# Optimization experiments

Measured on AMD Instinct MI355X. Metric: run time of the kernel, lower is better.

Reference implementation:

```python
import jax, jax.numpy as jnp
import numpy as np

N = 50000
E = 800000
IN_CH = 128
HID = 64
HEADS = 4
NEG_SLOPE_GAT = 0.2   # PyG GATConv default negative_slope
NEG_SLOPE_ACT = 0.01  # nn.LeakyReLU default
LN_EPS = 1e-5


def segment_softmax(logits, seg, num):
    # softmax over edges grouped by destination node (PyG softmax semantics)
    m = jax.ops.segment_max(logits, seg, num_segments=num)
    m = jnp.where(jnp.isfinite(m), m, 0.0)
    e = jnp.exp(logits - m[seg])
    s = jax.ops.segment_sum(e, seg, num_segments=num)
    return e / (s[seg] + 1e-16)


def gat_conv(x, edge_index, W, a_src, a_dst, b, heads, out_ch):
    n = x.shape[0]
    loop = jnp.arange(n)
    src = jnp.concatenate([edge_index[0], loop])  # message sources (x_j)
    dst = jnp.concatenate([edge_index[1], loop])  # aggregation targets (x_i)
    h = (x @ W).reshape(n, heads, out_ch)          # [N,H,C]
    alpha_src = (h * a_src).sum(-1)                # [N,H]
    alpha_dst = (h * a_dst).sum(-1)                # [N,H]
    alpha = alpha_src[src] + alpha_dst[dst]        # [E',H]
    alpha = jax.nn.leaky_relu(alpha, NEG_SLOPE_GAT)
    alpha = segment_softmax(alpha, dst, n)
    msg = h[src] * alpha[:, :, None]               # [E',H,C] gathered messages
    out = jax.ops.segment_sum(msg, dst, num_segments=n)  # [N,H,C]
    return out.reshape(n, heads * out_ch) + b


def layer_norm(x, gamma, beta):
    mu = x.mean(-1, keepdims=True)
    var = ((x - mu) ** 2).mean(-1, keepdims=True)
    return (x - mu) * jax.lax.rsqrt(var + LN_EPS) * gamma + beta


def setup_inputs() -> dict:
    key = jax.random.key(0)
    ks = jax.random.split(key, 12)
    d1 = HEADS * HID
    inp = {
        "x": jax.random.normal(ks[0], (N, IN_CH), dtype=jnp.float32),
        "edge_index": jax.random.randint(ks[1], (2, E), 0, N, dtype=jnp.int64),
        "W1": jax.random.normal(ks[2], (IN_CH, d1), dtype=jnp.float32) * 0.05,
        "a_src1": jax.random.normal(ks[3], (HEADS, HID), dtype=jnp.float32) * 0.1,
        "a_dst1": jax.random.normal(ks[4], (HEADS, HID), dtype=jnp.float32) * 0.1,
        "b1": jnp.zeros((d1,), dtype=jnp.float32),
        "gamma": jnp.ones((d1,), dtype=jnp.float32),
        "beta": jnp.zeros((d1,), dtype=jnp.float32),
        "W2": jax.random.normal(ks[5], (d1, HID), dtype=jnp.float32) * 0.05,
        "a_src2": jax.random.normal(ks[6], (1, HID), dtype=jnp.float32) * 0.1,
        "a_dst2": jax.random.normal(ks[7], (1, HID), dtype=jnp.float32) * 0.1,
        "b2": jnp.zeros((HID,), dtype=jnp.float32),
    }
    return inp


def reference(x, edge_index, W1, a_src1, a_dst1, b1, gamma, beta, W2, a_src2, a_dst2, b2):
    h = gat_conv(x, edge_index, W1, a_src1, a_dst1, b1, HEADS, HID)  # [N, H*HID]
    h = layer_norm(h, gamma, beta)
    h = jax.nn.leaky_relu(h, NEG_SLOPE_ACT)
    out = gat_conv(h, edge_index, W2, a_src2, a_dst2, b2, 1, HID)    # [N, HID]
    return out
```

## Files before the change

kernel.cpp:

```cpp
#include <hip/hip_runtime.h>
#include <hip/hip_bf16.h>

#define IN_CH 128
#define D1 256
#define HID 64
#define HEADS 4
#define SCAN_BLK 1024

typedef _Float16 h16;
typedef __attribute__((ext_vector_type(4))) _Float16 half4v;
typedef __attribute__((ext_vector_type(8))) _Float16 half8v;
typedef __attribute__((ext_vector_type(4))) float f32x4;

__device__ __forceinline__ float lrelu02(float v) { return v > 0.f ? v : 0.2f * v; }
__device__ __forceinline__ float lrelu001(float v) { return v > 0.f ? v : 0.01f * v; }

__global__ __launch_bounds__(256) void setup_kernel(const float* __restrict__ W1,
                                                    const float* __restrict__ W2,
                                                    const float* __restrict__ a_src1,
                                                    const float* __restrict__ a_dst1,
                                                    const float* __restrict__ a_src2,
                                                    const float* __restrict__ a_dst2,
                                                    const int* __restrict__ ei,
                                                    int* __restrict__ cnt,
                                                    h16* __restrict__ w1t,
                                                    h16* __restrict__ w2t,
                                                    int nE) {
    const int b = blockIdx.x;
    const int t = threadIdx.x;
    if (b == 0) {
        for (int k = 0; k < IN_CH; ++k) w1t[t * IN_CH + k] = (h16)W1[k * D1 + t];
    } else if (b == 1) {
        if (t < HID)
            for (int k = 0; k < D1; ++k) w2t[t * D1 + k] = (h16)W2[k * HID + t];
        for (int i = t; i < 14 * D1; i += 256) w2t[66 * D1 + i] = (h16)0.f;
    } else if (b == 2) {
        for (int o = t; o < 1024; o += 256) {
            int v = o >> 7, k = o & 127;
            int h = v & 3;
            const float* avec = (v >> 2) ? (a_dst1 + h * HID) : (a_src1 + h * HID);
            const float* wrow = W1 + k * D1 + h * HID;
            float s = 0.f;
            for (int c = 0; c < HID; ++c) s += wrow[c] * avec[c];
            w1t[(256 + v) * IN_CH + k] = (h16)s;
            w1t[(264 + v) * IN_CH + k] = (h16)0.f;
        }
    } else if (b == 3) {
        for (int o = t; o < 512; o += 256) {
            int v = o >> 8, k = o & 255;
            const float* avec = v ? a_dst2 : a_src2;
            const float* wrow = W2 + k * HID;
            float s = 0.f;
            for (int c = 0; c < HID; ++c) s += wrow[c] * avec[c];
            w2t[(64 + v) * D1 + k] = (h16)s;
        }
    } else {
        int e = (b - 4) * 256 + t;
        if (e < nE) atomicAdd(&cnt[ei[nE + e]], 1);
    }
}

__global__ __launch_bounds__(256) void scan1_kernel(const int* __restrict__ cnt,
                                                    int* __restrict__ pre,
                                                    int* __restrict__ blockSums, int n) {
    __shared__ int lds[256];
    const int t = threadIdx.x;
    const int base = blockIdx.x * SCAN_BLK + t * 4;
    int v0 = 0, v1 = 0, v2 = 0, v3 = 0;
    if (base + 0 < n) v0 = (cnt[base + 0] + 3) & ~3;
    if (base + 1 < n) v1 = (cnt[base + 1] + 3) & ~3;
    if (base + 2 < n) v2 = (cnt[base + 2] + 3) & ~3;
    if (base + 3 < n) v3 = (cnt[base + 3] + 3) & ~3;
    int s = v0 + v1 + v2 + v3;
    lds[t] = s;
    __syncthreads();
    for (int off = 1; off < 256; off <<= 1) {
        int x = 0;
        if (t >= off) x = lds[t - off];
        __syncthreads();
        if (t >= off) lds[t] += x;
        __syncthreads();
    }
    int excl = lds[t] - s;
    if (t == 255) blockSums[blockIdx.x] = lds[255];
    if (base + 0 < n) pre[base + 0] = excl;
    if (base + 1 < n) pre[base + 1] = excl + v0;
    if (base + 2 < n) pre[base + 2] = excl + v0 + v1;
    if (base + 3 < n) pre[base + 3] = excl + v0 + v1 + v2;
}

__global__ __launch_bounds__(256) void scan23_gemm1_kernel(
        int* __restrict__ pre, const int* __restrict__ blockSums,
        int* __restrict__ cursor, int* __restrict__ srcIdx,
        float* __restrict__ asad2, int n, int nbScan,
        const float* __restrict__ x, const h16* __restrict__ w1t,
        h16* __restrict__ h1, float* __restrict__ asad) {
    if (blockIdx.x < (unsigned)nbScan) {
        __shared__ int soff_s;
        const int t = threadIdx.x;
        if (t < 64) {
            int v = (t < (int)blockIdx.x && t < nbScan) ? blockSums[t] : 0;
            #pragma unroll
            for (int off = 1; off < 64; off <<= 1) v += __shfl_xor(v, off, 64);
            if (t == 0) soff_s = v;
        }
        __syncthreads();
        const int soff = soff_s;
        const int base = blockIdx.x * SCAN_BLK + t * 4;
        #pragma unroll
        for (int q = 0; q < 4; ++q) {
            int i = base + q;
            if (i < n) {
                int d = cursor[i];
                int v = pre[i] + soff;
                pre[i] = v;
                cursor[i] = v;
                int dp = (d + 3) & ~3;
                for (int p = d; p < dp; ++p) srcIdx[v + p] = n;
                if (i == n - 1) pre[n] = v + dp;
            }
        }
        if (blockIdx.x == 0 && t == 0) {
            asad2[(size_t)n * 2] = -1e30f;
            asad2[(size_t)n * 2 + 1] = -1e30f;
        }
        return;
    }
    const int bid = blockIdx.x - nbScan;
    const int wave = threadIdx.x >> 6, lane = threadIdx.x & 63;
    const int r = lane & 15, ksel = lane >> 4;
    const int rowBase = bid * 64 + wave * 16;
    const int row_a = rowBase + r;
    half8v a[4];
    if (row_a < n) {
        const float* xrow = x + (size_t)row_a * IN_CH + ksel * 8;
        #pragma unroll
        for (int kk = 0; kk < 4; ++kk) {
            float4 u = *(const float4*)(xrow + kk * 32);
            float4 v = *(const float4*)(xrow + kk * 32 + 4);
            half8v av;
            av[0] = (h16)u.x; av[1] = (h16)u.y; av[2] = (h16)u.z; av[3] = (h16)u.w;
            av[4] = (h16)v.x; av[5] = (h16)v.y; av[6] = (h16)v.z; av[7] = (h16)v.w;
            a[kk] = av;
        }
    } else {
        #pragma unroll
        for (int kk = 0; kk < 4; ++kk) a[kk] = (half8v){};
    }
    f32x4 acc[17];
    #pragma unroll
    for (int ct = 0; ct < 17; ++ct) acc[ct] = (f32x4){0.f, 0.f, 0.f, 0.f};
    #pragma unroll
    for (int ct = 0; ct < 17; ++ct) {
        const h16* wrow = w1t + (size_t)(ct * 16 + r) * IN_CH + ksel * 8;
        #pragma unroll
        for (int kk = 0; kk < 4; ++kk) {
            half8v b = *(const half8v*)(wrow + kk * 32);
            acc[ct] = __builtin_amdgcn_mfma_f32_16x16x32_f16(a[kk], b, acc[ct], 0, 0, 0);
        }
    }
    #pragma unroll
    for (int i = 0; i < 4; ++i) {
        int row = rowBase + ksel * 4 + i;
        if (row < n) {
            #pragma unroll
            for (int ct = 0; ct < 16; ++ct)
                h1[(size_t)row * D1 + ct * 16 + r] = (h16)acc[ct][i];
            if (r < 8) asad[(size_t)row * 8 + r] = acc[16][i];
        }
    }
}

__global__ __launch_bounds__(256) void scatter_ewt_kernel(const int* __restrict__ ei,
                                                          int* __restrict__ cursor,
                                                          const float* __restrict__ asad,
                                                          int* __restrict__ srcIdx,
                                                          h16* __restrict__ wE1, int nE) {
    int e = blockIdx.x * 256 + threadIdx.x;
    if (e >= nE) return;
    int src = ei[e];
    int dst = ei[nE + e];
    int pos = atomicAdd(&cursor[dst], 1);
    srcIdx[pos] = src;
    float4 as = *(const float4*)&asad[(size_t)src * 8];
    float4 ad = *(const float4*)&asad[(size_t)dst * 8 + 4];
    half4v w;
    w.x = (h16)expf(lrelu02(as.x + ad.x));
    w.y = (h16)expf(lrelu02(as.y + ad.y));
    w.z = (h16)expf(lrelu02(as.z + ad.z));
    w.w = (h16)expf(lrelu02(as.w + ad.w));
    *(half4v*)&wE1[(size_t)pos * 4] = w;
}

__global__ __launch_bounds__(256) void gemm2_mfma(const h16* __restrict__ hm,
                                                  const h16* __restrict__ w2t,
                                                  h16* __restrict__ h2,
                                                  float* __restrict__ asad2, int n) {
    const int wave = threadIdx.x >> 6, lane = threadIdx.x & 63;
    const int r = lane & 15, ksel = lane >> 4;
    const int rowBase = blockIdx.x * 64 + wave * 16;
    const h16* xrow = hm + (size_t)(rowBase + r) * D1 + ksel * 8;
    half8v a[8];
    #pragma unroll
    for (int kk = 0; kk < 8; ++kk) a[kk] = *(const half8v*)(xrow + kk * 32);
    f32x4 acc[5];
    #pragma unroll
    for (int ct = 0; ct < 5; ++ct) acc[ct] = (f32x4){0.f, 0.f, 0.f, 0.f};
    #pragma unroll
    for (int ct = 0; ct < 5; ++ct) {
        const h16* wrow = w2t + (size_t)(ct * 16 + r) * D1 + ksel * 8;
        #pragma unroll
        for (int kk = 0; kk < 8; ++kk) {
            half8v b = *(const half8v*)(wrow + kk * 32);
            acc[ct] = __builtin_amdgcn_mfma_f32_16x16x32_f16(a[kk], b, acc[ct], 0, 0, 0);
        }
    }
    #pragma unroll
    for (int i = 0; i < 4; ++i) {
        int row = rowBase + ksel * 4 + i;
        if (row < n) {
            #pragma unroll
            for (int ct = 0; ct < 4; ++ct)
                h2[(size_t)row * HID + ct * 16 + r] = (h16)acc[ct][i];
            if (r < 2) asad2[(size_t)row * 2 + r] = acc[4][i];
        }
    }
}

__global__ __launch_bounds__(256) void gather1_kernel(const h16* __restrict__ h1,
                                                      const float* __restrict__ asad,
                                                      const h16* __restrict__ wE1,
                                                      const int* __restrict__ rowStart,
                                                      const int* __restrict__ srcIdx,
                                                      const float* __restrict__ b1,
                                                      const float* __restrict__ gamma,
                                                      const float* __restrict__ beta,
                                                      h16* __restrict__ hmid,
                                                      int n, int npad) {
    const int lane = threadIdx.x & 63;
    const int node = (blockIdx.x * 256 + threadIdx.x) >> 6;
    if (node >= npad) return;
    if (node >= n) {
        half4v z = {};
        *(half4v*)&hmid[(size_t)node * D1 + lane * 4] = z;
        return;
    }
    const int hh = lane >> 4;
    const float wself = expf(lrelu02(asad[(size_t)node * 8 + hh] +
                                     asad[(size_t)node * 8 + 4 + hh]));
    half4v sv = *(const half4v*)&h1[(size_t)node * D1 + lane * 4];
    h16 wsh = (h16)wself;
    half4v acc = sv * (half4v){wsh, wsh, wsh, wsh};
    float den = wself;
    const int beg = rowStart[node], end = rowStart[node + 1];
    int j = beg;
    for (; j + 8 <= end; j += 8) {
        int4 ia = *(const int4*)&srcIdx[j];
        int4 ib = *(const int4*)&srcIdx[j + 4];
        h16 w0 = wE1[(size_t)(j + 0) * 4 + hh];
        h16 w1 = wE1[(size_t)(j + 1) * 4 + hh];
        h16 w2 = wE1[(size_t)(j + 2) * 4 + hh];
        h16 w3 = wE1[(size_t)(j + 3) * 4 + hh];
        h16 w4 = wE1[(size_t)(j + 4) * 4 + hh];
        h16 w5 = wE1[(size_t)(j + 5) * 4 + hh];
        h16 w6 = wE1[(size_t)(j + 6) * 4 + hh];
        h16 w7 = wE1[(size_t)(j + 7) * 4 + hh];
        half4v r0 = *(const half4v*)&h1[(size_t)ia.x * D1 + lane * 4];
        half4v r1 = *(const half4v*)&h1[(size_t)ia.y * D1 + lane * 4];
        half4v r2 = *(const half4v*)&h1[(size_t)ia.z * D1 + lane * 4];
        half4v r3 = *(const half4v*)&h1[(size_t)ia.w * D1 + lane * 4];
        half4v r4 = *(const half4v*)&h1[(size_t)ib.x * D1 + lane * 4];
        half4v r5 = *(const half4v*)&h1[(size_t)ib.y * D1 + lane * 4];
        half4v r6 = *(const half4v*)&h1[(size_t)ib.z * D1 + lane * 4];
        half4v r7 = *(const half4v*)&h1[(size_t)ib.w * D1 + lane * 4];
        acc += r0 * (half4v){w0, w0, w0, w0};
        acc += r1 * (half4v){w1, w1, w1, w1};
        acc += r2 * (half4v){w2, w2, w2, w2};
        acc += r3 * (half4v){w3, w3, w3, w3};
        acc += r4 * (half4v){w4, w4, w4, w4};
        acc += r5 * (half4v){w5, w5, w5, w5};
        acc += r6 * (half4v){w6, w6, w6, w6};
        acc += r7 * (half4v){w7, w7, w7, w7};
        den += (float)w0 + (float)w1 + (float)w2 + (float)w3
             + (float)w4 + (float)w5 + (float)w6 + (float)w7;
    }
    if (j < end) {
        int4 ia = *(const int4*)&srcIdx[j];
        h16 w0 = wE1[(size_t)(j + 0) * 4 + hh];
        h16 w1 = wE1[(size_t)(j + 1) * 4 + hh];
        h16 w2 = wE1[(size_t)(j + 2) * 4 + hh];
        h16 w3 = wE1[(size_t)(j + 3) * 4 + hh];
        half4v r0 = *(const half4v*)&h1[(size_t)ia.x * D1 + lane * 4];
        half4v r1 = *(const half4v*)&h1[(size_t)ia.y * D1 + lane * 4];
        half4v r2 = *(const half4v*)&h1[(size_t)ia.z * D1 + lane * 4];
        half4v r3 = *(const half4v*)&h1[(size_t)ia.w * D1 + lane * 4];
        acc += r0 * (half4v){w0, w0, w0, w0};
        acc += r1 * (half4v){w1, w1, w1, w1};
        acc += r2 * (half4v){w2, w2, w2, w2};
        acc += r3 * (half4v){w3, w3, w3, w3};
        den += (float)w0 + (float)w1 + (float)w2 + (float)w3;
    }
    float4 accf = make_float4((float)acc[0], (float)acc[1], (float)acc[2], (float)acc[3]);
    float inv = 1.f / (den + 1e-16f);
    float4 bv = *(const float4*)&b1[lane * 4];
    float4 y;
    y.x = accf.x * inv + bv.x; y.y = accf.y * inv + bv.y;
    y.z = accf.z * inv + bv.z; y.w = accf.w * inv + bv.w;
    float s = y.x + y.y + y.z + y.w;
    #pragma unroll
    for (int off = 1; off < 64; off <<= 1) s += __shfl_xor(s, off, 64);
    float mu = s * (1.f / 256.f);
    float4 dx;
    dx.x = y.x - mu; dx.y = y.y - mu; dx.z = y.z - mu; dx.w = y.w - mu;
    float sq = dx.x * dx.x + dx.y * dx.y + dx.z * dx.z + dx.w * dx.w;
    #pragma unroll
    for (int off = 1; off < 64; off <<= 1) sq += __shfl_xor(sq, off, 64);
    float rs = rsqrtf(sq * (1.f / 256.f) + 1e-5f);
    float4 g = *(const float4*)&gamma[lane * 4];
    float4 be = *(const float4*)&beta[lane * 4];
    half4v o;
    o.x = (h16)lrelu001(dx.x * rs * g.x + be.x);
    o.y = (h16)lrelu001(dx.y * rs * g.y + be.y);
    o.z = (h16)lrelu001(dx.z * rs * g.z + be.z);
    o.w = (h16)lrelu001(dx.w * rs * g.w + be.w);
    *(half4v*)&hmid[(size_t)node * D1 + lane * 4] = o;
}

__global__ __launch_bounds__(256) void gather2_kernel(const h16* __restrict__ h2,
                                                      const float* __restrict__ asad2,
                                                      const int* __restrict__ rowStart,
                                                      const int* __restrict__ srcIdx,
                                                      const float* __restrict__ b2,
                                                      float* __restrict__ out, int n) {
    const int lane = threadIdx.x & 63;
    const int node = (blockIdx.x * 256 + threadIdx.x) >> 6;
    if (node >= n) return;
    const int li = lane & 15, eh = lane >> 4;
    const int c0 = li * 4;
    const float ad_n = asad2[(size_t)node * 2 + 1];
    float acc[4] = {0.f, 0.f, 0.f, 0.f};
    float den = 0.f;
    if (eh == 0) {
        float w0 = expf(lrelu02(asad2[(size_t)node * 2] + ad_n));
        half4v sv = *(const half4v*)&h2[(size_t)node * HID + c0];
        #pragma unroll
        for (int i = 0; i < 4; ++i) acc[i] = (float)sv[i] * w0;
        den = w0;
    }
    const int beg = rowStart[node], end = rowStart[node + 1];
    int j = beg;
    for (; j + 8 <= end; j += 8) {
        int e0 = j + eh, e1 = j + 4 + eh;
        int s0 = srcIdx[e0], s1 = srcIdx[e1];
        float a0 = asad2[(size_t)s0 * 2], a1 = asad2[(size_t)s1 * 2];
        half4v r0 = *(const half4v*)&h2[(size_t)s0 * HID + c0];
        half4v r1 = *(const half4v*)&h2[(size_t)s1 * HID + c0];
        float w0 = expf(lrelu02(a0 + ad_n));
        float w1 = expf(lrelu02(a1 + ad_n));
        #pragma unroll
        for (int i = 0; i < 4; ++i) {
            acc[i] = fmaf((float)r0[i], w0, acc[i]);
            acc[i] = fmaf((float)r1[i], w1, acc[i]);
        }
        den += w0 + w1;
    }
    if (j < end) {
        int e = j + eh;
        int s = srcIdx[e];
        float w = expf(lrelu02(asad2[(size_t)s * 2] + ad_n));
        half4v r = *(const half4v*)&h2[(size_t)s * HID + c0];
        #pragma unroll
        for (int i = 0; i < 4; ++i) acc[i] = fmaf((float)r[i], w, acc[i]);
        den += w;
    }
    #pragma unroll
    for (int i = 0; i < 4; ++i) {
        acc[i] += __shfl_xor(acc[i], 32, 64);
        acc[i] += __shfl_xor(acc[i], 16, 64);
    }
    den += __shfl_xor(den, 32, 64);
    den += __shfl_xor(den, 16, 64);
    if (lane < 16) {
        float inv = 1.f / (den + 1e-16f);
        float4 bv = *(const float4*)&b2[c0];
        float4 o;
        o.x = acc[0] * inv + bv.x;
        o.y = acc[1] * inv + bv.y;
        o.z = acc[2] * inv + bv.z;
        o.w = acc[3] * inv + bv.w;
        *(float4*)&out[(size_t)node * HID + c0] = o;
    }
}

extern "C" void kernel_launch(void* const* d_in, const int* in_sizes, int n_in,
                              void* d_out, int out_size, void* d_ws, size_t ws_size,
                              hipStream_t stream) {
    const float* x      = (const float*)d_in[0];
    const int*   ei     = (const int*)d_in[1];
    const float* W1     = (const float*)d_in[2];
    const float* a_src1 = (const float*)d_in[3];
    const float* a_dst1 = (const float*)d_in[4];
    const float* b1     = (const float*)d_in[5];
    const float* gamma  = (const float*)d_in[6];
    const float* beta   = (const float*)d_in[7];
    const float* W2     = (const float*)d_in[8];
    const float* a_src2 = (const float*)d_in[9];
    const float* a_dst2 = (const float*)d_in[10];
    const float* b2     = (const float*)d_in[11];
    float* out = (float*)d_out;

    const int N = in_sizes[0] / IN_CH;
    const int E = in_sizes[1] / 2;
    const int NP = (N + 63) & ~63;
    const int Emax = E + 3 * N + 16;

    float* ws = (float*)d_ws;
    size_t off = 0;
    h16*   h1   = (h16*)(ws + off); off += (size_t)128 * (N + 1);
    h16*   hmid = (h16*)(ws + off); off += (size_t)128 * NP;
    h16*   h2   = (h16*)(ws + off); off += (size_t)32 * (N + 1);
    float* asad = ws + off;         off += (size_t)8 * N;
    float* asad2= ws + off;         off += (size_t)2 * (N + 1);
    int* rowStart  = (int*)(ws + off); off += N + 1;
    int* blockSums = (int*)(ws + off); off += 64;
    h16* w1t = (h16*)(ws + off); off += 17408;
    h16* w2t = (h16*)(ws + off); off += 10240;
    int* cursor = (int*)(ws + off); off += N;
    int* srcIdx = (int*)(ws + off); off += Emax;
    h16* wE1    = (h16*)(ws + off); off += (size_t)2 * Emax;
    const size_t memsetBytes = ((size_t)N + Emax) * 4 + (size_t)4 * Emax * 2;

    const int nodeBlocks  = (N + 3) / 4;
    const int nodeBlocksP = (NP + 3) / 4;
    const int nThreadBlocksE = (E + 255) / 256;
    const int scanBlocks = (N + SCAN_BLK - 1) / SCAN_BLK;

    hipMemsetAsync(cursor, 0, memsetBytes, stream);
    setup_kernel<<<4 + nThreadBlocksE, 256, 0, stream>>>(
        W1, W2, a_src1, a_dst1, a_src2, a_dst2, ei, cursor, w1t, w2t, E);
    scan1_kernel<<<scanBlocks, 256, 0, stream>>>(cursor, rowStart, blockSums, N);
    scan23_gemm1_kernel<<<scanBlocks + NP / 64, 256, 0, stream>>>(
        rowStart, blockSums, cursor, srcIdx, asad2, N, scanBlocks,
        x, w1t, h1, asad);
    scatter_ewt_kernel<<<nThreadBlocksE, 256, 0, stream>>>(ei, cursor, asad, srcIdx,
                                                           wE1, E);
    gather1_kernel<<<nodeBlocksP, 256, 0, stream>>>(h1, asad, wE1, rowStart, srcIdx,
                                                    b1, gamma, beta, hmid, N, NP);
    gemm2_mfma<<<NP / 64, 256, 0, stream>>>(hmid, w2t, h2, asad2, N);
    gather2_kernel<<<nodeBlocks, 256, 0, stream>>>(h2, asad2, rowStart, srcIdx,
                                                   b2, out, N);
}
```

Baseline: 257.5 us.

## Replace two-pass CSR prefix scan with wave-level atomic segment allocation

Drops the separate scan1 kernel and the block-sum pass. Each wave now does a local shuffle scan over padded degrees and reserves its range of edge slots with one atomicAdd on a global counter. Per-node end offsets go into a separate rowEnd array, because segments are no longer contiguous in node order. This removes one kernel launch and its dependency. In exchange, CSR segments are ordered nondeterministically, which may reduce locality in the gather kernels.

```diff
diff --git a/kernel.cpp b/kernel.cpp
--- a/kernel.cpp
+++ b/kernel.cpp
@@ -5,7 +5,6 @@
 #define D1 256
 #define HID 64
 #define HEADS 4
-#define SCAN_BLK 1024
 
 typedef _Float16 h16;
 typedef __attribute__((ext_vector_type(4))) _Float16 half4v;
@@ -60,64 +59,46 @@
     }
 }
 
-__global__ __launch_bounds__(256) void scan1_kernel(const int* __restrict__ cnt,
-                                                    int* __restrict__ pre,
-                                                    int* __restrict__ blockSums, int n) {
-    __shared__ int lds[256];
-    const int t = threadIdx.x;
-    const int base = blockIdx.x * SCAN_BLK + t * 4;
-    int v0 = 0, v1 = 0, v2 = 0, v3 = 0;
-    if (base + 0 < n) v0 = (cnt[base + 0] + 3) & ~3;
-    if (base + 1 < n) v1 = (cnt[base + 1] + 3) & ~3;
-    if (base + 2 < n) v2 = (cnt[base + 2] + 3) & ~3;
-    if (base + 3 < n) v3 = (cnt[base + 3] + 3) & ~3;
-    int s = v0 + v1 + v2 + v3;
-    lds[t] = s;
-    __syncthreads();
-    for (int off = 1; off < 256; off <<= 1) {
-        int x = 0;
-        if (t >= off) x = lds[t - off];
-        __syncthreads();
-        if (t >= off) lds[t] += x;
-        __syncthreads();
-    }
-    int excl = lds[t] - s;
-    if (t == 255) blockSums[blockIdx.x] = lds[255];
-    if (base + 0 < n) pre[base + 0] = excl;
-    if (base + 1 < n) pre[base + 1] = excl + v0;
-    if (base + 2 < n) pre[base + 2] = excl + v0 + v1;
-    if (base + 3 < n) pre[base + 3] = excl + v0 + v1 + v2;
-}
-
-__global__ __launch_bounds__(256) void scan23_gemm1_kernel(
-        int* __restrict__ pre, const int* __restrict__ blockSums,
-        int* __restrict__ cursor, int* __restrict__ srcIdx,
-        float* __restrict__ asad2, int n, int nbScan,
+__global__ __launch_bounds__(256) void assign_gemm1_kernel(
+        int* __restrict__ cursor,
+        int* __restrict__ rowStart, int* __restrict__ rowEnd,
+        int* __restrict__ srcIdx, int* __restrict__ gcount,
+        float* __restrict__ asad2, int n, int nbAssign,
         const float* __restrict__ x, const h16* __restrict__ w1t,
         h16* __restrict__ h1, float* __restrict__ asad) {
-    if (blockIdx.x < (unsigned)nbScan) {
-        __shared__ int soff_s;
+    if (blockIdx.x < (unsigned)nbAssign) {
         const int t = threadIdx.x;
-        if (t < 64) {
-            int v = (t < (int)blockIdx.x && t < nbScan) ? blockSums[t] : 0;
-            #pragma unroll
-            for (int off = 1; off < 64; off <<= 1) v += __shfl_xor(v, off, 64);
-            if (t == 0) soff_s = v;
-        }
-        __syncthreads();
-        const int soff = soff_s;
-        const int base = blockIdx.x * SCAN_BLK + t * 4;
+        const int lane = t & 63;
+        const int base = blockIdx.x * 1024 + t * 4;
+        int d[4], dp[4];
+        int tsum = 0;
+        #pragma unroll
+        for (int q = 0; q < 4; ++q) {
+            int i = base + q;
+            d[q] = (i < n) ? cursor[i] : 0;
+            dp[q] = (d[q] + 3) & ~3;
+            tsum += dp[q];
+        }
+        int incl = tsum;
+        #pragma unroll
+        for (int off = 1; off < 64; off <<= 1) {
+            int y = __shfl_up(incl, off, 64);
+            if (lane >= off) incl += y;
+        }
+        int total = __shfl(incl, 63, 64);
+        int wbase = 0;
+        if (lane == 63) wbase = atomicAdd(gcount, total);
+        wbase = __shfl(wbase, 63, 64);
+        int start = wbase + (incl - tsum);
         #pragma unroll
         for (int q = 0; q < 4; ++q) {
             int i = base + q;
             if (i < n) {
-                int d = cursor[i];
-                int v = pre[i] + soff;
-                pre[i] = v;
-                cursor[i] = v;
-                int dp = (d + 3) & ~3;
-                for (int p = d; p < dp; ++p) srcIdx[v + p] = n;
-                if (i == n - 1) pre[n] = v + dp;
+                rowStart[i] = start;
+                cursor[i] = start;
+                rowEnd[i] = start + dp[q];
+                for (int p = d[q]; p < dp[q]; ++p) srcIdx[start + p] = n;
+                start += dp[q];
             }
         }
         if (blockIdx.x == 0 && t == 0) {
@@ -126,7 +107,7 @@
         }
         return;
     }
-    const int bid = blockIdx.x - nbScan;
+    const int bid = blockIdx.x - nbAssign;
     const int wave = threadIdx.x >> 6, lane = threadIdx.x & 63;
     const int r = lane & 15, ksel = lane >> 4;
     const int rowBase = bid * 64 + wave * 16;
@@ -231,6 +212,7 @@
                                                       const float* __restrict__ asad,
                                                       const h16* __restrict__ wE1,
                                                       const int* __restrict__ rowStart,
+                                                      const int* __restrict__ rowEnd,
                                                       const int* __restrict__ srcIdx,
                                                       const float* __restrict__ b1,
                                                       const float* __restrict__ gamma,
@@ -252,7 +234,7 @@
     h16 wsh = (h16)wself;
     half4v acc = sv * (half4v){wsh, wsh, wsh, wsh};
     float den = wself;
-    const int beg = rowStart[node], end = rowStart[node + 1];
+    const int beg = rowStart[node], end = rowEnd[node];
     int j = beg;
     for (; j + 8 <= end; j += 8) {
         int4 ia = *(const int4*)&srcIdx[j];
@@ -329,6 +311,7 @@
 __global__ __launch_bounds__(256) void gather2_kernel(const h16* __restrict__ h2,
                                                       const float* __restrict__ asad2,
                                                       const int* __restrict__ rowStart,
+                                                      const int* __restrict__ rowEnd,
                                                       const int* __restrict__ srcIdx,
                                                       const float* __restrict__ b2,
                                                       float* __restrict__ out, int n) {
@@ -347,7 +330,7 @@
         for (int i = 0; i < 4; ++i) acc[i] = (float)sv[i] * w0;
         den = w0;
     }
-    const int beg = rowStart[node], end = rowStart[node + 1];
+    const int beg = rowStart[node], end = rowEnd[node];
     int j = beg;
     for (; j + 8 <= end; j += 8) {
         int e0 = j + eh, e1 = j + 4 + eh;
@@ -421,32 +404,32 @@
     h16*   h2   = (h16*)(ws + off); off += (size_t)32 * (N + 1);
     float* asad = ws + off;         off += (size_t)8 * N;
     float* asad2= ws + off;         off += (size_t)2 * (N + 1);
-    int* rowStart  = (int*)(ws + off); off += N + 1;
-    int* blockSums = (int*)(ws + off); off += 64;
+    int* rowStart  = (int*)(ws + off); off += N;
+    int* rowEnd    = (int*)(ws + off); off += N;
     h16* w1t = (h16*)(ws + off); off += 17408;
     h16* w2t = (h16*)(ws + off); off += 10240;
+    int* gcount = (int*)(ws + off); off += 1;
     int* cursor = (int*)(ws + off); off += N;
     int* srcIdx = (int*)(ws + off); off += Emax;
     h16* wE1    = (h16*)(ws + off); off += (size_t)2 * Emax;
-    const size_t memsetBytes = ((size_t)N + Emax) * 4 + (size_t)4 * Emax * 2;
+    const size_t memsetBytes = ((size_t)1 + N + Emax) * 4 + (size_t)4 * Emax * 2;
 
     const int nodeBlocks  = (N + 3) / 4;
     const int nodeBlocksP = (NP + 3) / 4;
     const int nThreadBlocksE = (E + 255) / 256;
-    const int scanBlocks = (N + SCAN_BLK - 1) / SCAN_BLK;
-
-    hipMemsetAsync(cursor, 0, memsetBytes, stream);
+    const int nbAssign = (N + 1023) / 1024;
+
+    hipMemsetAsync(gcount, 0, memsetBytes, stream);
     setup_kernel<<<4 + nThreadBlocksE, 256, 0, stream>>>(
         W1, W2, a_src1, a_dst1, a_src2, a_dst2, ei, cursor, w1t, w2t, E);
-    scan1_kernel<<<scanBlocks, 256, 0, stream>>>(cursor, rowStart, blockSums, N);
-    scan23_gemm1_kernel<<<scanBlocks + NP / 64, 256, 0, stream>>>(
-        rowStart, blockSums, cursor, srcIdx, asad2, N, scanBlocks,
+    assign_gemm1_kernel<<<nbAssign + NP / 64, 256, 0, stream>>>(
+        cursor, rowStart, rowEnd, srcIdx, gcount, asad2, N, nbAssign,
         x, w1t, h1, asad);
     scatter_ewt_kernel<<<nThreadBlocksE, 256, 0, stream>>>(ei, cursor, asad, srcIdx,
                                                            wE1, E);
-    gather1_kernel<<<nodeBlocksP, 256, 0, stream>>>(h1, asad, wE1, rowStart, srcIdx,
-                                                    b1, gamma, beta, hmid, N, NP);
+    gather1_kernel<<<nodeBlocksP, 256, 0, stream>>>(h1, asad, wE1, rowStart, rowEnd,
+                                                    srcIdx, b1, gamma, beta, hmid, N, NP);
     gemm2_mfma<<<NP / 64, 256, 0, stream>>>(hmid, w2t, h2, asad2, N);
-    gather2_kernel<<<nodeBlocks, 256, 0, stream>>>(h2, asad2, rowStart, srcIdx,
+    gather2_kernel<<<nodeBlocks, 256, 0, stream>>>(h2, asad2, rowStart, rowEnd, srcIdx,
                                                    b2, out, N);
 }
```

Measured after the change: 258.3 us. Within noise of the previous version (+0.3%).
